# Optimization experiments

Hardware: AMD Instinct MI355X
Metric: run time of the kernel (lower is better)

The kernel has to match this reference:

```python
import jax, jax.numpy as jnp
import numpy as np
from jax import lax

B_SZ = 64
D_MODEL = 768
D_INNER = 1536   # expand * d_model
D_STATE = 16
D_CONV = 4
DT_RANK = 48     # ceil(768/16)
ROWS, COLS = 16, 16
L = ROWS * COLS
LN_EPS = 1e-5


def setup_inputs() -> dict:
    key = jax.random.key(0)
    ks = jax.random.split(key, 16)
    def nrm(k, shape, s):
        return jax.random.normal(k, shape, jnp.float32) * s
    # A_log init as in Mamba: log(arange(1..d_state)) tiled over d_inner
    A_log = jnp.log(jnp.tile(jnp.arange(1, D_STATE + 1, dtype=jnp.float32)[None, :], (D_INNER, 1)))
    # dt bias init: inverse-softplus of dt ~ LogUniform(1e-3, 1e-1)
    def dt_bias_init(k):
        u = jax.random.uniform(k, (D_INNER,), jnp.float32)
        dt = jnp.exp(u * (np.log(0.1) - np.log(0.001)) + np.log(0.001))
        return dt + jnp.log(-jnp.expm1(-dt))
    dt_std = DT_RANK ** -0.5
    return {
        "hidden_states": jax.random.normal(ks[0], (B_SZ, L, D_MODEL), jnp.float32),
        "in_proj_w": nrm(ks[1], (2 * D_INNER, D_MODEL), 0.02),
        "conv_w": nrm(ks[2], (D_INNER, D_CONV), 0.2),
        "conv_bias": nrm(ks[3], (D_INNER,), 0.1),
        "conv_w_b": nrm(ks[4], (D_INNER, D_CONV), 0.2),
        "conv_bias_b": nrm(ks[5], (D_INNER,), 0.1),
        "x_proj_w": nrm(ks[6], (DT_RANK + 2 * D_STATE, D_INNER), 0.02),
        "x_proj_w_b": nrm(ks[7], (DT_RANK + 2 * D_STATE, D_INNER), 0.02),
        "dt_proj_w": jax.random.uniform(ks[8], (D_INNER, DT_RANK), jnp.float32, -dt_std, dt_std),
        "dt_proj_w_b": jax.random.uniform(ks[9], (D_INNER, DT_RANK), jnp.float32, -dt_std, dt_std),
        "dt_bias": dt_bias_init(ks[10]),
        "dt_bias_b": dt_bias_init(ks[11]),
        "A_log": A_log,
        "A_b_log": A_log,
        "Dp": jnp.ones((D_INNER,), jnp.float32),
        "Dp_b": jnp.ones((D_INNER,), jnp.float32),
        "ln_gamma": jnp.ones((D_INNER,), jnp.float32),
        "ln_beta": jnp.zeros((D_INNER,), jnp.float32),
        "out_proj_w": nrm(ks[12], (D_MODEL, D_INNER), 0.02),
    }


def _causal_conv_silu(x, w, b):
    # x: (B, D, L); depthwise causal conv (left-pad K-1) + SiLU
    y = lax.conv_general_dilated(x, w[:, None, :], (1,), [(D_CONV - 1, 0)],
                                 dimension_numbers=("NCH", "OIH", "NCH"),
                                 feature_group_count=D_INNER)
    return jax.nn.silu(y + b[None, :, None])


def _selective_scan(u, dt, A_log, Bm, Cm, dt_bias):
    # u, dt: (B, D, Lr); Bm, Cm: (B, N, Lr)
    A = -jnp.exp(A_log)                                     # (D, N)
    delta = jax.nn.softplus(dt + dt_bias[None, :, None])    # (B, D, Lr)
    dA = jnp.exp(jnp.einsum("bdl,dn->lbdn", delta, A))     # (Lr, B, D, N)
    dBu = jnp.einsum("bdl,bnl,bdl->lbdn", delta, Bm, u)    # (Lr, B, D, N)
    C_l = jnp.moveaxis(Cm, -1, 0)                           # (Lr, B, N)
    def step(h, inp):
        dA_t, dBu_t, C_t = inp
        h = dA_t * h + dBu_t
        return h, jnp.einsum("bdn,bn->bd", h, C_t)
    h0 = jnp.zeros(dA.shape[1:], dA.dtype)
    _, ys = lax.scan(step, h0, (dA, dBu, C_l))
    return jnp.moveaxis(ys, 0, -1)                          # (B, D, Lr)


def _direction(x, conv_w, conv_bias, x_proj_w, dt_proj_w, dt_bias, A_log, Dp):
    xc = _causal_conv_silu(x, conv_w, conv_bias)            # (B, D, L)
    x_comp = xc.reshape(-1, D_INNER, ROWS, COLS).mean(axis=3)  # (B, D, ROWS)
    x_dbl = jnp.einsum("bdl,ed->ble", x_comp, x_proj_w)    # (B, ROWS, R+2N)
    dt, Bm, Cm = jnp.split(x_dbl, [DT_RANK, DT_RANK + D_STATE], axis=-1)
    dt = jnp.einsum("blr,dr->bdl", dt, dt_proj_w)          # (B, D, ROWS)
    Bm = jnp.moveaxis(Bm, 1, 2)                             # (B, N, ROWS)
    Cm = jnp.moveaxis(Cm, 1, 2)
    y = _selective_scan(x_comp, dt, A_log, Bm, Cm, dt_bias)
    return jnp.repeat(y, COLS, axis=2) + Dp[None, :, None] * xc  # (B, D, L)


def reference(hidden_states, in_proj_w, conv_w, conv_bias, conv_w_b, conv_bias_b,
              x_proj_w, x_proj_w_b, dt_proj_w, dt_proj_w_b, dt_bias, dt_bias_b,
              A_log, A_b_log, Dp, Dp_b, ln_gamma, ln_beta, out_proj_w):
    xz = jnp.einsum("bld,ed->bel", hidden_states, in_proj_w)  # (B, 2*Di, L)
    x, z = jnp.split(xz, 2, axis=1)
    out_f = _direction(x, conv_w, conv_bias, x_proj_w, dt_proj_w, dt_bias, A_log, Dp)
    out_b = _direction(x[:, :, ::-1], conv_w_b, conv_bias_b, x_proj_w_b, dt_proj_w_b, dt_bias_b, A_b_log, Dp_b)
    comb = jnp.moveaxis((out_f + out_b[:, :, ::-1]) * 0.5, 1, 2)  # (B, L, Di)
    mu = comb.mean(-1, keepdims=True)
    var = comb.var(-1, keepdims=True)
    normed = (comb - mu) * lax.rsqrt(var + LN_EPS) * ln_gamma + ln_beta
    gated = normed * jax.nn.silu(jnp.moveaxis(z, 1, 2))
    return jnp.einsum("bld,od->blo", gated, out_proj_w)       # (B, L, d_model)
```

## Files before the change

kernel.cpp:

```cpp
#include <hip/hip_runtime.h>
#include <cstdint>
#include <cstddef>

typedef __bf16 bf16_t;
typedef __attribute__((ext_vector_type(2))) __bf16 bf16x2;
typedef __attribute__((ext_vector_type(8))) __bf16 bf16x8;
typedef __attribute__((ext_vector_type(4))) float f32x4;
typedef __attribute__((ext_vector_type(2))) float f32x2;

#define NB     64
#define LSEQ   256
#define DM     768
#define DI     1536
#define NSTATE 16
#define NROWS  16
#define RANK   48

#define BF16_PROBE 0x3F803F80u

__device__ __forceinline__ float bf2f(bf16_t v) { return (float)v; }

__device__ __forceinline__ float ldp(const void* p, size_t i, bool isbf) {
  return isbf ? (float)((const bf16_t*)p)[i] : ((const float*)p)[i];
}

__device__ __forceinline__ float silu_f(float x) {
  const float e = __expf(-fabsf(x));
  return (x >= 0.f) ? (x / (1.f + e)) : (x * e / (1.f + e));
}

__device__ __forceinline__ void async16(const bf16_t* g, bf16_t* l) {
  __builtin_amdgcn_global_load_lds(
      (const __attribute__((address_space(1))) void*)g,
      (__attribute__((address_space(3))) void*)l, 16, 0, 0);
}

__global__ __launch_bounds__(256) void cvt_kernel(
    const void* __restrict__ in, bf16_t* __restrict__ out, int n8,
    const uint32_t* __restrict__ probe)
{
  const int i = blockIdx.x * 256 + threadIdx.x;
  if (i >= n8) return;
  if (probe[0] == BF16_PROBE) {
    ((bf16x8*)out)[i] = ((const bf16x8*)in)[i];
  } else {
    const float* f = (const float*)in + (size_t)i * 8;
    f32x4 lo = *(const f32x4*)f, hi = *(const f32x4*)(f + 4);
    ((bf16x8*)out)[i] = (bf16x8){(bf16_t)lo.x, (bf16_t)lo.y, (bf16_t)lo.z, (bf16_t)lo.w,
                                 (bf16_t)hi.x, (bf16_t)hi.y, (bf16_t)hi.z, (bf16_t)hi.w};
  }
}

#define LDS_IDX(ab, db, half) (((ab) << 2) + ((db) << 1) + (half))

#define STAGE(ab, db, half, kt) do {                                          \
    const int _kt = ((kt) < NT) ? (kt) : (NT - 1);                            \
    const bf16_t* _g = (ab) ? B : A;                                          \
    const size_t _rb = ((ab) ? bn : bm) + (size_t)((half) * 128);             \
    bf16_t* _l = &sm[LDS_IDX(ab, db, half)][0];                               \
    _Pragma("unroll")                                                         \
    for (int _j = 0; _j < 2; _j++) {                                          \
      const int _c = wave * 2 + _j;                                           \
      async16(_g + (_rb + _c * 8 + srow) * (size_t)K + (size_t)_kt * 64 + scol,\
              _l + _c * 512);                                                 \
    }                                                                         \
  } while (0)

#define LOAD_A(db, mg) do {                                                   \
    _Pragma("unroll")                                                         \
    for (int _t = 0; _t < 2; _t++) {                                          \
      const int _mt = (mg) * 2 + _t;                                          \
      const int _lr = _mt * 32 + wm * 16 + r;                                 \
      const bf16_t* _b = &sm[LDS_IDX(0, db, _mt >> 2)][(_lr & 127) * 64];     \
      _Pragma("unroll")                                                       \
      for (int _s = 0; _s < 2; _s++)                                          \
        af[_t][_s] = *(const bf16x8*)&_b[(((_s * 4 + quad) ^ r7) * 8)];       \
    }                                                                         \
  } while (0)

#define LOAD_B(db) do {                                                       \
    _Pragma("unroll")                                                         \
    for (int _nt = 0; _nt < 4; _nt++) {                                       \
      const int _lr = _nt * 64 + wn * 16 + r;                                 \
      const bf16_t* _b = &sm[LDS_IDX(1, db, _lr >> 7)][(_lr & 127) * 64];     \
      _Pragma("unroll")                                                       \
      for (int _s = 0; _s < 2; _s++)                                          \
        bfr[_nt][_s] = *(const bf16x8*)&_b[(((_s * 4 + quad) ^ r7) * 8)];     \
    }                                                                         \
  } while (0)

#define MFMA16(mg) do {                                                       \
    __builtin_amdgcn_s_setprio(1);                                            \
    _Pragma("unroll")                                                         \
    for (int _t = 0; _t < 2; _t++)                                            \
    _Pragma("unroll")                                                         \
    for (int _nt = 0; _nt < 4; _nt++)                                         \
    _Pragma("unroll")                                                         \
    for (int _s = 0; _s < 2; _s++)                                            \
      acc[(mg) * 2 + _t][_nt] = __builtin_amdgcn_mfma_f32_16x16x32_bf16(      \
          af[_t][_s], bfr[_nt][_s], acc[(mg) * 2 + _t][_nt], 0, 0, 0);        \
    __builtin_amdgcn_s_setprio(0);                                            \
  } while (0)

#define BAR()    __builtin_amdgcn_s_barrier()
#define WAITL0() asm volatile("s_waitcnt lgkmcnt(0)" ::: "memory")
#define WAITV6() asm volatile("s_waitcnt vmcnt(6)" ::: "memory")

__global__ __launch_bounds__(512, 2) void gemm256_kernel(
    const bf16_t* __restrict__ A, const bf16_t* __restrict__ B,
    void* __restrict__ C, int M, int N, int K, int mode,
    bf16_t* __restrict__ xb)
{
  __shared__ bf16_t sm[8][8192];
  const int tid  = threadIdx.x;
  const int wave = tid >> 6, lane = tid & 63;
  const int wm = wave >> 2, wn = wave & 3;
  const int r = lane & 15, quad = lane >> 4, r7 = lane & 7;
  const int srow = lane >> 3;
  const int scol = ((lane & 7) ^ srow) * 8;
  const int NT = K >> 6;

  const int nwg  = gridDim.x * gridDim.y;
  const int orig = blockIdx.y * gridDim.x + blockIdx.x;
  const int swz  = (orig & 7) * (nwg >> 3) + (orig >> 3);
  const size_t bm = (size_t)(swz / gridDim.x) * 256;
  const size_t bn = (size_t)(swz % gridDim.x) * 256;

  f32x4 acc[8][4];
#pragma unroll
  for (int i = 0; i < 8; i++)
#pragma unroll
    for (int j = 0; j < 4; j++) acc[i][j] = (f32x4){0.f, 0.f, 0.f, 0.f};

  bf16x8 af[2][2];
  bf16x8 bfr[4][2];

  STAGE(1, 0, 0, 0);  STAGE(1, 0, 1, 0);  STAGE(0, 0, 0, 0);  STAGE(0, 0, 1, 0);
  asm volatile("s_waitcnt vmcnt(4)" ::: "memory");
  STAGE(1, 1, 0, 1);  STAGE(1, 1, 1, 1);  STAGE(0, 1, 0, 1);
  WAITV6();
  BAR();

  const int NP = NT >> 1;
  for (int i = 0; i < NP; ++i) {
    const int t1 = 2 * i + 1, t2 = 2 * i + 2, t3 = 2 * i + 3;
    LOAD_B(0); LOAD_A(0, 0); STAGE(0, 1, 1, t1);
    BAR(); WAITL0(); MFMA16(0); BAR();

    LOAD_A(0, 1); STAGE(1, 0, 0, t2);
    BAR(); WAITL0(); MFMA16(1); BAR();

    LOAD_A(0, 2); STAGE(1, 0, 1, t2);
    BAR(); WAITL0(); MFMA16(2); BAR();

    LOAD_A(0, 3); STAGE(0, 0, 0, t2);
    WAITV6();
    BAR(); WAITL0(); MFMA16(3); BAR();

    LOAD_B(1); LOAD_A(1, 0); STAGE(0, 0, 1, t2);
    BAR(); WAITL0(); MFMA16(0); BAR();

    LOAD_A(1, 1); STAGE(1, 1, 0, t3);
    BAR(); WAITL0(); MFMA16(1); BAR();

    LOAD_A(1, 2); STAGE(1, 1, 1, t3);
    BAR(); WAITL0(); MFMA16(2); BAR();

    LOAD_A(1, 3); STAGE(0, 1, 0, t3);
    WAITV6();
    BAR(); WAITL0(); MFMA16(3); BAR();
  }

  const int col16 = lane & 15;
  const int rb4 = quad * 4;

  if (mode == 0) {
#pragma unroll
    for (int mt = 0; mt < 8; mt++)
#pragma unroll
      for (int nt = 0; nt < 4; nt++)
#pragma unroll
        for (int v = 0; v < 4; v++) {
          const size_t m = bm + mt * 32 + wm * 16 + rb4 + v;
          const size_t n = bn + nt * 64 + wn * 16 + col16;
          ((float*)C)[m * (size_t)N + n] = acc[mt][nt][v];
        }
  } else {
    bf16_t* dst = (bn < (size_t)DI) ? xb : (bf16_t*)C;
    const size_t cb0 = (bn < (size_t)DI) ? bn : bn - DI;
#pragma unroll
    for (int mt = 0; mt < 8; mt++)
#pragma unroll
      for (int nt = 0; nt < 4; nt++)
#pragma unroll
        for (int v = 0; v < 4; v++) {
          const size_t m = bm + mt * 32 + wm * 16 + rb4 + v;
          dst[m * DI + cb0 + nt * 64 + wn * 16 + col16] = (bf16_t)acc[mt][nt][v];
        }
  }
}

__global__ __launch_bounds__(256) void conv_kernel(
    const bf16_t* __restrict__ xb,
    const void* __restrict__ cw_f, const void* __restrict__ cb_f,
    const void* __restrict__ cw_b, const void* __restrict__ cb_b,
    bf16_t* __restrict__ xc_f, bf16_t* __restrict__ xc_b,
    float* __restrict__ comp_f, float* __restrict__ comp_b,
    const uint32_t* __restrict__ probe)
{
  const bool isbf = (probe[0] == BF16_PROBE);
  int bi = blockIdx.x;
  const int chunk = bi & 3;
  bi >>= 2;
  const int b = bi / 3;
  const int pblk = bi % 3;
  const int d0 = (pblk * 256 + threadIdx.x) * 2;
  const int lr0 = chunk * 64;

  const float wf0a = ldp(cw_f, (size_t)d0 * 4 + 0, isbf),
              wf1a = ldp(cw_f, (size_t)d0 * 4 + 1, isbf),
              wf2a = ldp(cw_f, (size_t)d0 * 4 + 2, isbf),
              wf3a = ldp(cw_f, (size_t)d0 * 4 + 3, isbf);
  const float wf0c = ldp(cw_f, (size_t)(d0 + 1) * 4 + 0, isbf),
              wf1c = ldp(cw_f, (size_t)(d0 + 1) * 4 + 1, isbf),
              wf2c = ldp(cw_f, (size_t)(d0 + 1) * 4 + 2, isbf),
              wf3c = ldp(cw_f, (size_t)(d0 + 1) * 4 + 3, isbf);
  const float wb0a = ldp(cw_b, (size_t)d0 * 4 + 0, isbf),
              wb1a = ldp(cw_b, (size_t)d0 * 4 + 1, isbf),
              wb2a = ldp(cw_b, (size_t)d0 * 4 + 2, isbf),
              wb3a = ldp(cw_b, (size_t)d0 * 4 + 3, isbf);
  const float wb0c = ldp(cw_b, (size_t)(d0 + 1) * 4 + 0, isbf),
              wb1c = ldp(cw_b, (size_t)(d0 + 1) * 4 + 1, isbf),
              wb2c = ldp(cw_b, (size_t)(d0 + 1) * 4 + 2, isbf),
              wb3c = ldp(cw_b, (size_t)(d0 + 1) * 4 + 3, isbf);
  const float bfa = ldp(cb_f, d0, isbf), bfc = ldp(cb_f, d0 + 1, isbf);
  const float bba = ldp(cb_b, d0, isbf), bbc = ldp(cb_b, d0 + 1, isbf);

  const bf16_t* xrow = xb + (size_t)b * LSEQ * DI + d0;

  float t0a = 0.f, t1a = 0.f, t2a = 0.f, t3a = 0.f;
  float t0c = 0.f, t1c = 0.f, t2c = 0.f, t3c = 0.f;
  if (lr0 > 0) {
    bf16x2 v;
    v = *(const bf16x2*)&xrow[(size_t)(lr0 - 3) * DI]; t1a = (float)v.x; t1c = (float)v.y;
    v = *(const bf16x2*)&xrow[(size_t)(lr0 - 2) * DI]; t2a = (float)v.x; t2c = (float)v.y;
    v = *(const bf16x2*)&xrow[(size_t)(lr0 - 1) * DI]; t3a = (float)v.x; t3c = (float)v.y;
  }

  float sfa = 0.f, sfc = 0.f;
  float sba = 0.f, sbc = 0.f;
  for (int l = lr0; l < lr0 + 67; ++l) {
    float xa = 0.f, xcv = 0.f;
    if (l < LSEQ) {
      bf16x2 v = *(const bf16x2*)&xrow[(size_t)l * DI];
      xa = (float)v.x; xcv = (float)v.y;
    }
    t0a = t1a; t1a = t2a; t2a = t3a; t3a = xa;
    t0c = t1c; t1c = t2c; t2c = t3c; t3c = xcv;

    if (l < lr0 + 64) {
      const float ya = silu_f(bfa + wf0a * t0a + wf1a * t1a + wf2a * t2a + wf3a * t3a);
      const float yc = silu_f(bfc + wf0c * t0c + wf1c * t1c + wf2c * t2c + wf3c * t3c);
      *(bf16x2*)&xc_f[((size_t)b * LSEQ + l) * DI + d0] = (bf16x2){(bf16_t)ya, (bf16_t)yc};
      sfa += ya; sfc += yc;
      if ((l & 15) == 15) {
        *(f32x2*)&comp_f[((size_t)b * NROWS + (l >> 4)) * DI + d0] =
            (f32x2){sfa * (1.f / 16.f), sfc * (1.f / 16.f)};
        sfa = 0.f; sfc = 0.f;
      }
    }
    if (l >= lr0 + 3) {
      const int j = 258 - l;
      const float ya = silu_f(bba + wb0a * t3a + wb1a * t2a + wb2a * t1a + wb3a * t0a);
      const float yc = silu_f(bbc + wb0c * t3c + wb1c * t2c + wb2c * t1c + wb3c * t0c);
      *(bf16x2*)&xc_b[((size_t)b * LSEQ + j) * DI + d0] = (bf16x2){(bf16_t)ya, (bf16_t)yc};
      sba += ya; sbc += yc;
      if ((j & 15) == 0) {
        *(f32x2*)&comp_b[((size_t)b * NROWS + (j >> 4)) * DI + d0] =
            (f32x2){sba * (1.f / 16.f), sbc * (1.f / 16.f)};
        sba = 0.f; sbc = 0.f;
      }
    }
  }
}

__global__ __launch_bounds__(256) void xproj_kernel(
    const float* __restrict__ comp_f, const float* __restrict__ comp_b,
    const void* __restrict__ w_f, const void* __restrict__ w_b,
    float* __restrict__ xd_f, float* __restrict__ xd_b,
    const uint32_t* __restrict__ probe)
{
  const bool isbf = (probe[0] == BF16_PROBE);
  const int dir = blockIdx.y;
  const int row = blockIdx.x;
  const float* comp = dir ? comp_b : comp_f;
  const void* W = dir ? w_b : w_f;
  float* out = dir ? xd_b : xd_f;

  __shared__ float xrow[DI];
  for (int i = threadIdx.x; i < DI; i += 256) xrow[i] = comp[(size_t)row * DI + i];
  __syncthreads();

  const int wave = threadIdx.x >> 6, lane = threadIdx.x & 63;
  for (int oo = 0; oo < 20; ++oo) {
    const int o = wave * 20 + oo;
    float s = 0.f;
#pragma unroll
    for (int j = 0; j < 24; ++j) {
      const int k = lane + 64 * j;
      s += xrow[k] * ldp(W, (size_t)o * DI + k, isbf);
    }
    for (int off = 32; off; off >>= 1) s += __shfl_down(s, off);
    if (lane == 0) out[(size_t)row * 80 + o] = s;
  }
}

__global__ __launch_bounds__(256) void scan_kernel(
    const float* __restrict__ xd_fg, const float* __restrict__ xd_bg,
    const float* comp_f, const float* comp_b,
    const void* __restrict__ dtw_f, const void* __restrict__ dtw_b,
    const void* __restrict__ dtb_f, const void* __restrict__ dtb_b,
    const void* __restrict__ Al_f, const void* __restrict__ Al_b,
    float* y_fg, float* y_bg,
    const uint32_t* __restrict__ probe)
{
  const bool isbf = (probe[0] == BF16_PROBE);
  const int dir = blockIdx.y;
  const int b = blockIdx.x / 6;
  const int d = (blockIdx.x % 6) * 256 + threadIdx.x;
  const float* xd_g = dir ? xd_bg : xd_fg;
  const float* comp = dir ? comp_b : comp_f;
  const void* dtw = dir ? dtw_b : dtw_f;
  const void* dtb = dir ? dtb_b : dtb_f;
  const void* Al  = dir ? Al_b : Al_f;
  float* y = dir ? y_bg : y_fg;

  __shared__ float xd[NROWS * 80];
  for (int i = threadIdx.x; i < NROWS * 80; i += 256) xd[i] = xd_g[(size_t)b * (NROWS * 80) + i];
  __syncthreads();

  float dt[NROWS];
#pragma unroll
  for (int l = 0; l < NROWS; l++) dt[l] = 0.f;
  for (int r = 0; r < RANK; r++) {
    const float w = ldp(dtw, (size_t)d * RANK + r, isbf);
#pragma unroll
    for (int l = 0; l < NROWS; l++) dt[l] += xd[l * 80 + r] * w;
  }

  float A[NSTATE];
#pragma unroll
  for (int n = 0; n < NSTATE; n++) A[n] = -__expf(ldp(Al, (size_t)d * NSTATE + n, isbf));
  const float bias = ldp(dtb, d, isbf);

  float h[NSTATE];
#pragma unroll
  for (int n = 0; n < NSTATE; n++) h[n] = 0.f;

  for (int l = 0; l < NROWS; l++) {
    const float u = comp[((size_t)b * NROWS + l) * DI + d];
    const float dv = dt[l] + bias;
    const float delta = (dv > 15.f) ? dv : log1pf(__expf(dv));
    const float du = delta * u;
    float yv = 0.f;
#pragma unroll
    for (int n = 0; n < NSTATE; n++) {
      const float hn = __expf(delta * A[n]) * h[n] + du * xd[l * 80 + RANK + n];
      h[n] = hn;
      yv += hn * xd[l * 80 + RANK + NSTATE + n];
    }
    y[((size_t)b * NROWS + l) * DI + d] = yv;
  }
}

__global__ __launch_bounds__(256) void combine_kernel(
    const float* __restrict__ y_f, const float* __restrict__ y_b,
    bf16_t* xcg_f,
    const bf16_t* __restrict__ xc_b,
    const bf16_t* __restrict__ zb,
    const void* __restrict__ Dp, const void* __restrict__ Dp_b,
    const void* __restrict__ gamma, const void* __restrict__ beta,
    const uint32_t* __restrict__ probe)
{
  const bool isbf = (probe[0] == BF16_PROBE);
  const int m = blockIdx.x;
  const int b = m >> 8, l = m & 255;
  const int lr = LSEQ - 1 - l;
  const int tid = threadIdx.x;

  float v[6];
  float sum = 0.f, sq = 0.f;
#pragma unroll
  for (int i = 0; i < 6; i++) {
    const int d = tid + i * 256;
    const float cf = bf2f(xcg_f[((size_t)b * LSEQ + l) * DI + d]);
    const float cb = bf2f(xc_b[((size_t)b * LSEQ + lr) * DI + d]);
    const float vf = y_f[((size_t)b * NROWS + (l >> 4)) * DI + d] + ldp(Dp, d, isbf) * cf;
    const float vb = y_b[((size_t)b * NROWS + (lr >> 4)) * DI + d] + ldp(Dp_b, d, isbf) * cb;
    const float c = 0.5f * (vf + vb);
    v[i] = c; sum += c; sq += c * c;
  }
  for (int off = 32; off; off >>= 1) {
    sum += __shfl_down(sum, off);
    sq  += __shfl_down(sq, off);
  }
  __shared__ float rs[4], rq[4];
  if ((tid & 63) == 0) { rs[tid >> 6] = sum; rq[tid >> 6] = sq; }
  __syncthreads();
  const float S  = rs[0] + rs[1] + rs[2] + rs[3];
  const float SQ = rq[0] + rq[1] + rq[2] + rq[3];
  const float mu = S * (1.f / (float)DI);
  const float var = fmaxf(SQ * (1.f / (float)DI) - mu * mu, 0.f);
  const float rstd = rsqrtf(var + 1e-5f);
#pragma unroll
  for (int i = 0; i < 6; i++) {
    const int d = tid + i * 256;
    const float nrm = (v[i] - mu) * rstd * ldp(gamma, d, isbf) + ldp(beta, d, isbf);
    const float z = bf2f(zb[(size_t)m * DI + d]);
    xcg_f[(size_t)m * DI + d] = (bf16_t)(nrm * silu_f(z));
  }
}

extern "C" void kernel_launch(void* const* d_in, const int* in_sizes, int n_in,
                              void* d_out, int out_size, void* d_ws, size_t ws_size,
                              hipStream_t stream)
{
  (void)in_sizes; (void)n_in; (void)out_size; (void)ws_size;
  const void* H     = d_in[0];
  const void* Win   = d_in[1];
  const void* cw_f  = d_in[2];
  const void* cb_f  = d_in[3];
  const void* cw_b  = d_in[4];
  const void* cb_b  = d_in[5];
  const void* xpw_f = d_in[6];
  const void* xpw_b = d_in[7];
  const void* dtw_f = d_in[8];
  const void* dtw_b = d_in[9];
  const void* dtb_f = d_in[10];
  const void* dtb_b = d_in[11];
  const void* Al_f  = d_in[12];
  const void* Al_b  = d_in[13];
  const void* Dp    = d_in[14];
  const void* Dp_b  = d_in[15];
  const void* gam   = d_in[16];
  const void* bet   = d_in[17];
  const void* Wout  = d_in[18];
  const uint32_t* probe = (const uint32_t*)d_in[14];

  const size_t M = (size_t)NB * LSEQ;
  char* ws = (char*)d_ws;
  bf16_t* zb    = (bf16_t*)ws;  ws += M * DI * sizeof(bf16_t);
  bf16_t* xb    = (bf16_t*)ws;  ws += M * DI * sizeof(bf16_t);
  bf16_t* xc_f  = (bf16_t*)ws;  ws += M * DI * sizeof(bf16_t);
  bf16_t* xc_b  = (bf16_t*)ws;  ws += M * DI * sizeof(bf16_t);
  float* comp_f = (float*)ws;   ws += (size_t)NB * NROWS * DI * sizeof(float);
  float* comp_b = (float*)ws;   ws += (size_t)NB * NROWS * DI * sizeof(float);
  float* xd_f   = (float*)ws;   ws += (size_t)NB * NROWS * 80 * sizeof(float);
  float* xd_b   = (float*)ws;   ws += (size_t)NB * NROWS * 80 * sizeof(float);
  bf16_t* Hb    = (bf16_t*)ws;  ws += M * DM * sizeof(bf16_t);
  bf16_t* Winb  = (bf16_t*)ws;  ws += (size_t)(2 * DI) * DM * sizeof(bf16_t);
  bf16_t* Woutb = (bf16_t*)ws;  ws += (size_t)DM * DI * sizeof(bf16_t);

  cvt_kernel<<<(int)((M * DM / 8 + 255) / 256), 256, 0, stream>>>(H, Hb, (int)(M * DM / 8), probe);
  cvt_kernel<<<(2 * DI * DM / 8 + 255) / 256, 256, 0, stream>>>(Win, Winb, 2 * DI * DM / 8, probe);
  cvt_kernel<<<(DM * DI / 8 + 255) / 256, 256, 0, stream>>>(Wout, Woutb, DM * DI / 8, probe);

  gemm256_kernel<<<dim3(2 * DI / 256, M / 256), 512, 0, stream>>>(
      Hb, Winb, zb, (int)M, 2 * DI, DM, 1, xb);

  conv_kernel<<<dim3(768), 256, 0, stream>>>(
      xb, cw_f, cb_f, cw_b, cb_b, xc_f, xc_b, comp_f, comp_b, probe);

  xproj_kernel<<<dim3(NB * NROWS, 2), 256, 0, stream>>>(
      comp_f, comp_b, xpw_f, xpw_b, xd_f, xd_b, probe);

  scan_kernel<<<dim3(NB * (DI / 256), 2), 256, 0, stream>>>(
      xd_f, xd_b, comp_f, comp_b, dtw_f, dtw_b, dtb_f, dtb_b, Al_f, Al_b,
      comp_f, comp_b, probe);

  combine_kernel<<<dim3(NB * LSEQ), 256, 0, stream>>>(
      comp_f, comp_b, xc_f, xc_b, zb, Dp, Dp_b, gam, bet, probe);

  gemm256_kernel<<<dim3(DM / 256, M / 256), 512, 0, stream>>>(
      xc_f, Woutb, d_out, (int)M, DM, DI, 0, nullptr);
}
```

Baseline: 482.7 us.

## Recompute causal conv in combine kernel instead of storing xc buffers

The conv kernel no longer writes the full-length forward and backward convolved activations. It now only produces the pooled row means. The combine kernel recomputes both causal convolutions from xb with a sliding window over 16-row chunks, handling 4 channels per thread with 384 threads. It then does LayerNorm and gating and writes to a separate gated buffer. A small kernel also pre-transposes dt_proj weights so the scan reads them coalesced. This removes two large bf16 writes and reads of M×DI elements, at the cost of extra conv arithmetic and one barrier per row in combine.

```diff
diff --git a/kernel.cpp b/kernel.cpp
--- a/kernel.cpp
+++ b/kernel.cpp
@@ -4,6 +4,7 @@
 
 typedef __bf16 bf16_t;
 typedef __attribute__((ext_vector_type(2))) __bf16 bf16x2;
+typedef __attribute__((ext_vector_type(4))) __bf16 bf16x4;
 typedef __attribute__((ext_vector_type(8))) __bf16 bf16x8;
 typedef __attribute__((ext_vector_type(4))) float f32x4;
 typedef __attribute__((ext_vector_type(2))) float f32x2;
@@ -49,6 +50,17 @@
     ((bf16x8*)out)[i] = (bf16x8){(bf16_t)lo.x, (bf16_t)lo.y, (bf16_t)lo.z, (bf16_t)lo.w,
                                  (bf16_t)hi.x, (bf16_t)hi.y, (bf16_t)hi.z, (bf16_t)hi.w};
   }
+}
+
+__global__ __launch_bounds__(256) void dtwt_kernel(
+    const void* __restrict__ dtw, float* __restrict__ out,
+    const uint32_t* __restrict__ probe)
+{
+  const bool isbf = (probe[0] == BF16_PROBE);
+  const int i = blockIdx.x * 256 + threadIdx.x;
+  if (i >= RANK * DI) return;
+  const int r = i / DI, d = i - r * DI;
+  out[i] = ldp(dtw, (size_t)d * RANK + r, isbf);
 }
 
 #define LDS_IDX(ab, db, half) (((ab) << 2) + ((db) << 1) + (half))
@@ -200,11 +212,10 @@
   }
 }
 
-__global__ __launch_bounds__(256) void conv_kernel(
+__global__ __launch_bounds__(256) void pool_kernel(
     const bf16_t* __restrict__ xb,
     const void* __restrict__ cw_f, const void* __restrict__ cb_f,
     const void* __restrict__ cw_b, const void* __restrict__ cb_b,
-    bf16_t* __restrict__ xc_f, bf16_t* __restrict__ xc_b,
     float* __restrict__ comp_f, float* __restrict__ comp_b,
     const uint32_t* __restrict__ probe)
 {
@@ -261,7 +272,6 @@
     if (l < lr0 + 64) {
       const float ya = silu_f(bfa + wf0a * t0a + wf1a * t1a + wf2a * t2a + wf3a * t3a);
       const float yc = silu_f(bfc + wf0c * t0c + wf1c * t1c + wf2c * t2c + wf3c * t3c);
-      *(bf16x2*)&xc_f[((size_t)b * LSEQ + l) * DI + d0] = (bf16x2){(bf16_t)ya, (bf16_t)yc};
       sfa += ya; sfc += yc;
       if ((l & 15) == 15) {
         *(f32x2*)&comp_f[((size_t)b * NROWS + (l >> 4)) * DI + d0] =
@@ -273,7 +283,6 @@
       const int j = 258 - l;
       const float ya = silu_f(bba + wb0a * t3a + wb1a * t2a + wb2a * t1a + wb3a * t0a);
       const float yc = silu_f(bbc + wb0c * t3c + wb1c * t2c + wb2c * t1c + wb3c * t0c);
-      *(bf16x2*)&xc_b[((size_t)b * LSEQ + j) * DI + d0] = (bf16x2){(bf16_t)ya, (bf16_t)yc};
       sba += ya; sbc += yc;
       if ((j & 15) == 0) {
         *(f32x2*)&comp_b[((size_t)b * NROWS + (j >> 4)) * DI + d0] =
@@ -318,7 +327,7 @@
 __global__ __launch_bounds__(256) void scan_kernel(
     const float* __restrict__ xd_fg, const float* __restrict__ xd_bg,
     const float* comp_f, const float* comp_b,
-    const void* __restrict__ dtw_f, const void* __restrict__ dtw_b,
+    const float* __restrict__ dtwT_f, const float* __restrict__ dtwT_b,
     const void* __restrict__ dtb_f, const void* __restrict__ dtb_b,
     const void* __restrict__ Al_f, const void* __restrict__ Al_b,
     float* y_fg, float* y_bg,
@@ -330,7 +339,7 @@
   const int d = (blockIdx.x % 6) * 256 + threadIdx.x;
   const float* xd_g = dir ? xd_bg : xd_fg;
   const float* comp = dir ? comp_b : comp_f;
-  const void* dtw = dir ? dtw_b : dtw_f;
+  const float* dtwT = dir ? dtwT_b : dtwT_f;
   const void* dtb = dir ? dtb_b : dtb_f;
   const void* Al  = dir ? Al_b : Al_f;
   float* y = dir ? y_bg : y_fg;
@@ -343,7 +352,7 @@
 #pragma unroll
   for (int l = 0; l < NROWS; l++) dt[l] = 0.f;
   for (int r = 0; r < RANK; r++) {
-    const float w = ldp(dtw, (size_t)d * RANK + r, isbf);
+    const float w = dtwT[(size_t)r * DI + d];
 #pragma unroll
     for (int l = 0; l < NROWS; l++) dt[l] += xd[l * 80 + r] * w;
   }
@@ -373,51 +382,110 @@
   }
 }
 
-__global__ __launch_bounds__(256) void combine_kernel(
+__global__ __launch_bounds__(384) void combine_kernel(
     const float* __restrict__ y_f, const float* __restrict__ y_b,
-    bf16_t* xcg_f,
-    const bf16_t* __restrict__ xc_b,
-    const bf16_t* __restrict__ zb,
+    const bf16_t* __restrict__ xb, const bf16_t* __restrict__ zb,
+    bf16_t* __restrict__ gated,
+    const void* __restrict__ cw_f, const void* __restrict__ cb_f,
+    const void* __restrict__ cw_b, const void* __restrict__ cb_b,
     const void* __restrict__ Dp, const void* __restrict__ Dp_b,
     const void* __restrict__ gamma, const void* __restrict__ beta,
     const uint32_t* __restrict__ probe)
 {
   const bool isbf = (probe[0] == BF16_PROBE);
-  const int m = blockIdx.x;
-  const int b = m >> 8, l = m & 255;
-  const int lr = LSEQ - 1 - l;
+  const int blk = blockIdx.x;
+  const int b = blk >> 4, g = blk & 15;
+  const int l0 = g * 16;
   const int tid = threadIdx.x;
-
-  float v[6];
-  float sum = 0.f, sq = 0.f;
-#pragma unroll
-  for (int i = 0; i < 6; i++) {
-    const int d = tid + i * 256;
-    const float cf = bf2f(xcg_f[((size_t)b * LSEQ + l) * DI + d]);
-    const float cb = bf2f(xc_b[((size_t)b * LSEQ + lr) * DI + d]);
-    const float vf = y_f[((size_t)b * NROWS + (l >> 4)) * DI + d] + ldp(Dp, d, isbf) * cf;
-    const float vb = y_b[((size_t)b * NROWS + (lr >> 4)) * DI + d] + ldp(Dp_b, d, isbf) * cb;
-    const float c = 0.5f * (vf + vb);
-    v[i] = c; sum += c; sq += c * c;
-  }
-  for (int off = 32; off; off >>= 1) {
-    sum += __shfl_down(sum, off);
-    sq  += __shfl_down(sq, off);
-  }
-  __shared__ float rs[4], rq[4];
-  if ((tid & 63) == 0) { rs[tid >> 6] = sum; rq[tid >> 6] = sq; }
-  __syncthreads();
-  const float S  = rs[0] + rs[1] + rs[2] + rs[3];
-  const float SQ = rq[0] + rq[1] + rq[2] + rq[3];
-  const float mu = S * (1.f / (float)DI);
-  const float var = fmaxf(SQ * (1.f / (float)DI) - mu * mu, 0.f);
-  const float rstd = rsqrtf(var + 1e-5f);
-#pragma unroll
-  for (int i = 0; i < 6; i++) {
-    const int d = tid + i * 256;
-    const float nrm = (v[i] - mu) * rstd * ldp(gamma, d, isbf) + ldp(beta, d, isbf);
-    const float z = bf2f(zb[(size_t)m * DI + d]);
-    xcg_f[(size_t)m * DI + d] = (bf16_t)(nrm * silu_f(z));
+  const int wave = tid >> 6, lane = tid & 63;
+  const int d0 = tid * 4;
+
+  float wf[4][4], wb_[4][4], cbf[4], cbb[4], dp[4], db[4], gm[4], bt[4];
+  float yfv[4], ybv[4];
+#pragma unroll
+  for (int c = 0; c < 4; c++) {
+    const int d = d0 + c;
+#pragma unroll
+    for (int i = 0; i < 4; i++) {
+      wf[c][i]  = ldp(cw_f, (size_t)d * 4 + i, isbf);
+      wb_[c][i] = ldp(cw_b, (size_t)d * 4 + i, isbf);
+    }
+    cbf[c] = ldp(cb_f, d, isbf);  cbb[c] = ldp(cb_b, d, isbf);
+    dp[c]  = ldp(Dp, d, isbf);    db[c]  = ldp(Dp_b, d, isbf);
+    gm[c]  = ldp(gamma, d, isbf); bt[c]  = ldp(beta, d, isbf);
+    yfv[c] = y_f[((size_t)b * NROWS + (l0 >> 4)) * DI + d];
+    ybv[c] = y_b[((size_t)b * NROWS + (15 - (l0 >> 4))) * DI + d];
+  }
+
+  const bf16_t* xrow = xb + (size_t)b * LSEQ * DI + d0;
+  const bf16_t* zrow = zb + (size_t)b * LSEQ * DI + d0;
+  bf16_t* grow = gated + (size_t)b * LSEQ * DI + d0;
+
+  float W[7][4];
+#pragma unroll
+  for (int j = 0; j < 6; j++) {
+    const int l = l0 - 3 + j;
+    if (l >= 0) {
+      const bf16x4 v = *(const bf16x4*)&xrow[(size_t)l * DI];
+#pragma unroll
+      for (int c = 0; c < 4; c++) W[j][c] = (float)v[c];
+    } else {
+#pragma unroll
+      for (int c = 0; c < 4; c++) W[j][c] = 0.f;
+    }
+  }
+
+  __shared__ float rs[2][6], rq[2][6];
+
+  for (int l = l0; l < l0 + 16; ++l) {
+    const int lf = l + 3;
+    if (lf < LSEQ) {
+      const bf16x4 v = *(const bf16x4*)&xrow[(size_t)lf * DI];
+#pragma unroll
+      for (int c = 0; c < 4; c++) W[6][c] = (float)v[c];
+    } else {
+#pragma unroll
+      for (int c = 0; c < 4; c++) W[6][c] = 0.f;
+    }
+
+    float v[4];
+    float sum = 0.f, sq = 0.f;
+#pragma unroll
+    for (int c = 0; c < 4; c++) {
+      const float cf = silu_f(cbf[c] + wf[c][0] * W[0][c] + wf[c][1] * W[1][c] +
+                              wf[c][2] * W[2][c] + wf[c][3] * W[3][c]);
+      const float cbv = silu_f(cbb[c] + wb_[c][0] * W[6][c] + wb_[c][1] * W[5][c] +
+                               wb_[c][2] * W[4][c] + wb_[c][3] * W[3][c]);
+      const float cc = 0.5f * ((yfv[c] + dp[c] * cf) + (ybv[c] + db[c] * cbv));
+      v[c] = cc; sum += cc; sq += cc * cc;
+    }
+    for (int off = 32; off; off >>= 1) {
+      sum += __shfl_down(sum, off);
+      sq  += __shfl_down(sq, off);
+    }
+    const int par = l & 1;
+    if (lane == 0) { rs[par][wave] = sum; rq[par][wave] = sq; }
+    __syncthreads();
+    float S = 0.f, SQ = 0.f;
+#pragma unroll
+    for (int w = 0; w < 6; w++) { S += rs[par][w]; SQ += rq[par][w]; }
+    const float mu = S * (1.f / (float)DI);
+    const float var = fmaxf(SQ * (1.f / (float)DI) - mu * mu, 0.f);
+    const float rstd = rsqrtf(var + 1e-5f);
+
+    const bf16x4 zv = *(const bf16x4*)&zrow[(size_t)l * DI];
+    bf16x4 outv;
+#pragma unroll
+    for (int c = 0; c < 4; c++) {
+      const float nrm = (v[c] - mu) * rstd * gm[c] + bt[c];
+      outv[c] = (bf16_t)(nrm * silu_f((float)zv[c]));
+    }
+    *(bf16x4*)&grow[(size_t)l * DI] = outv;
+
+#pragma unroll
+    for (int j = 0; j < 6; j++)
+#pragma unroll
+      for (int c = 0; c < 4; c++) W[j][c] = W[j + 1][c];
   }
 }
 
@@ -451,8 +519,7 @@
   char* ws = (char*)d_ws;
   bf16_t* zb    = (bf16_t*)ws;  ws += M * DI * sizeof(bf16_t);
   bf16_t* xb    = (bf16_t*)ws;  ws += M * DI * sizeof(bf16_t);
-  bf16_t* xc_f  = (bf16_t*)ws;  ws += M * DI * sizeof(bf16_t);
-  bf16_t* xc_b  = (bf16_t*)ws;  ws += M * DI * sizeof(bf16_t);
+  bf16_t* gated = (bf16_t*)ws;  ws += M * DI * sizeof(bf16_t);
   float* comp_f = (float*)ws;   ws += (size_t)NB * NROWS * DI * sizeof(float);
   float* comp_b = (float*)ws;   ws += (size_t)NB * NROWS * DI * sizeof(float);
   float* xd_f   = (float*)ws;   ws += (size_t)NB * NROWS * 80 * sizeof(float);
@@ -460,27 +527,32 @@
   bf16_t* Hb    = (bf16_t*)ws;  ws += M * DM * sizeof(bf16_t);
   bf16_t* Winb  = (bf16_t*)ws;  ws += (size_t)(2 * DI) * DM * sizeof(bf16_t);
   bf16_t* Woutb = (bf16_t*)ws;  ws += (size_t)DM * DI * sizeof(bf16_t);
+  float* dtwT_f = (float*)ws;   ws += (size_t)RANK * DI * sizeof(float);
+  float* dtwT_b = (float*)ws;   ws += (size_t)RANK * DI * sizeof(float);
 
   cvt_kernel<<<(int)((M * DM / 8 + 255) / 256), 256, 0, stream>>>(H, Hb, (int)(M * DM / 8), probe);
   cvt_kernel<<<(2 * DI * DM / 8 + 255) / 256, 256, 0, stream>>>(Win, Winb, 2 * DI * DM / 8, probe);
   cvt_kernel<<<(DM * DI / 8 + 255) / 256, 256, 0, stream>>>(Wout, Woutb, DM * DI / 8, probe);
+  dtwt_kernel<<<(RANK * DI + 255) / 256, 256, 0, stream>>>(dtw_f, dtwT_f, probe);
+  dtwt_kernel<<<(RANK * DI + 255) / 256, 256, 0, stream>>>(dtw_b, dtwT_b, probe);
 
   gemm256_kernel<<<dim3(2 * DI / 256, M / 256), 512, 0, stream>>>(
       Hb, Winb, zb, (int)M, 2 * DI, DM, 1, xb);
 
-  conv_kernel<<<dim3(768), 256, 0, stream>>>(
-      xb, cw_f, cb_f, cw_b, cb_b, xc_f, xc_b, comp_f, comp_b, probe);
+  pool_kernel<<<dim3(768), 256, 0, stream>>>(
+      xb, cw_f, cb_f, cw_b, cb_b, comp_f, comp_b, probe);
 
   xproj_kernel<<<dim3(NB * NROWS, 2), 256, 0, stream>>>(
       comp_f, comp_b, xpw_f, xpw_b, xd_f, xd_b, probe);
 
   scan_kernel<<<dim3(NB * (DI / 256), 2), 256, 0, stream>>>(
-      xd_f, xd_b, comp_f, comp_b, dtw_f, dtw_b, dtb_f, dtb_b, Al_f, Al_b,
+      xd_f, xd_b, comp_f, comp_b, dtwT_f, dtwT_b, dtb_f, dtb_b, Al_f, Al_b,
       comp_f, comp_b, probe);
 
-  combine_kernel<<<dim3(NB * LSEQ), 256, 0, stream>>>(
-      comp_f, comp_b, xc_f, xc_b, zb, Dp, Dp_b, gam, bet, probe);
+  combine_kernel<<<dim3(NB * NROWS), 384, 0, stream>>>(
+      comp_f, comp_b, xb, zb, gated,
+      cw_f, cb_f, cw_b, cb_b, Dp, Dp_b, gam, bet, probe);
 
   gemm256_kernel<<<dim3(DM / 256, M / 256), 512, 0, stream>>>(
-      xc_f, Woutb, d_out, (int)M, DM, DI, 0, nullptr);
-}
+      gated, Woutb, d_out, (int)M, DM, DI, 0, nullptr);
+}
```

Result: slower. 565.7 us (+17.2%).
